# Performance work log

Hardware: AMD Instinct MI355X
Metric: run time of the kernel (lower is better)

## Reference

```python
import jax, jax.numpy as jnp
import numpy as np

Lx, Ly, D, B = 6, 6, 3, 16
SIGMA = 0.5  # keeps the 36-tensor contraction magnitude in fp32 range


def _slice_config(T, s):
    # T: [Lx, Ly, D,D,D,D, 2,2,2,2,2]; bond axes (u,d,l,r), phys axes (self, up, down, left, right)
    sg = s.reshape(Lx, Ly)
    sp = jnp.pad(sg, 1)  # out-of-grid neighbors -> index 0
    ix, iy = jnp.meshgrid(jnp.arange(Lx), jnp.arange(Ly), indexing='ij')
    p = sg
    pu = sp[ix, iy + 1]      # neighbor (x-1, y)
    pd = sp[ix + 2, iy + 1]  # neighbor (x+1, y)
    pl = sp[ix + 1, iy]      # neighbor (x, y-1)
    pr = sp[ix + 1, iy + 2]  # neighbor (x, y+1)
    # advanced indexing: result [Lx, Ly, D, D, D, D] with bond axes (u, d, l, r)
    return T[ix, iy, :, :, :, :, p, pu, pd, pl, pr]


def _amplitude(T, s):
    # exact boundary contraction from ymin (no truncation), equals full .contract()
    A = _slice_config(T, s)            # [Lx, Ly, u, d, l, r]
    Bnd = A[:, 0, :, :, 0, :]          # cap dangling left bonds: [Lx, u, d, r]
    for y in range(1, Ly):
        C = A[:, y]                    # [Lx, u, d, l, r]
        Bnd = jnp.einsum('xabl,xudlr->xaubdr', Bnd, C)
        Bnd = Bnd.reshape(Lx, Bnd.shape[1] * Bnd.shape[2],
                          Bnd.shape[3] * Bnd.shape[4], D)
    M = Bnd[:, :, :, 0]                # cap dangling right bonds: [Lx, chi, chi]
    v = M[0, 0]                        # cap top boundary bond (index 0 of product bond)
    for xx in range(1, Lx):
        v = v @ M[xx]                  # vector-matrix chain down the boundary MPS
    return v[0]                        # cap bottom boundary bond


def setup_inputs() -> dict:
    key = jax.random.key(0)
    kT, kx = jax.random.split(key)
    T = jax.random.normal(kT, (Lx, Ly, D, D, D, D, 2, 2, 2, 2, 2), dtype=jnp.float32) * SIGMA
    x = jax.random.randint(kx, (B, Lx * Ly), 0, 2, dtype=jnp.int32)
    return {"x": x, "T": T}


def reference(x, T):
    # batched amplitudes: [B]
    return jax.vmap(lambda s: _amplitude(T, s))(x)
```

## Files before the change

kernel.cpp:

```cpp
#include <hip/hip_runtime.h>


constexpr int SITE_STRIDE = 81 * 32;

__device__ __forceinline__ int calc_sidx(const int* __restrict__ xs, int base, int s) {
    const int i = s / 6, j = s - (s / 6) * 6;
    const int p  = xs[base + s];
    const int pu = (i > 0) ? xs[base + s - 6] : 0;
    const int pd = (i < 5) ? xs[base + s + 6] : 0;
    const int pl = (j > 0) ? xs[base + s - 1] : 0;
    const int pr = (j < 5) ? xs[base + s + 1] : 0;
    return (((p * 2 + pu) * 2 + pd) * 2 + pl) * 2 + pr;
}

template <int U>
__device__ __forceinline__ void fused2(int lt, const float* __restrict__ Win,
                                       float* __restrict__ Wout,
                                       const float* __restrict__ A1,
                                       const float* __restrict__ A2,
                                       int SS, int SO) {
    if (lt >= 243) return;
    const int D  = lt / (3 * U);
    const int rem = lt - D * 3 * U;
    const int o1 = rem / U;
    const int ur = rem - o1 * U;
    const float* Wb = Win + D * 27 * U + ur;
    float win[3][3][3];
    #pragma unroll
    for (int l = 0; l < 3; ++l)
        #pragma unroll
        for (int s = 0; s < 3; ++s)
            #pragma unroll
            for (int m = 0; m < 3; ++m)
                win[l][s][m] = Wb[((l * 9 + s * 3 + m) * U)];
    float tt[3][3];
    #pragma unroll
    for (int r1 = 0; r1 < 3; ++r1)
        #pragma unroll
        for (int m = 0; m < 3; ++m) {
            float acc = 0.f;
            #pragma unroll
            for (int s = 0; s < 3; ++s)
                #pragma unroll
                for (int l = 0; l < 3; ++l)
                    acc += win[l][s][m] * A1[s * SS + o1 * SO + l * 3 + r1];
            tt[r1][m] = acc;
        }
    float* Wo = Wout + (D * 3 + o1) * 9 * U + ur;
    #pragma unroll
    for (int o2 = 0; o2 < 3; ++o2)
        #pragma unroll
        for (int r2 = 0; r2 < 3; ++r2) {
            float acc = 0.f;
            #pragma unroll
            for (int m = 0; m < 3; ++m)
                #pragma unroll
                for (int r1 = 0; r1 < 3; ++r1)
                    acc += tt[r1][m] * A2[m * SS + o2 * SO + r1 * 3 + r2];
            Wo[(o2 * 3 + r2) * U] = acc;
        }
}

__global__ __launch_bounds__(512)
void peps_amp_kernel(const int* __restrict__ xs, const float* __restrict__ T,
                     float* __restrict__ out) {
    __shared__ float A[36 * 81];
    __shared__ float Vsh[2][729];
    __shared__ float Wsh[2][2][2187];
    __shared__ float Pm[2][3][81];
    __shared__ float red[8];

    const int b = blockIdx.x;
    const int t = threadIdx.x;
    const int half = t >> 8;
    const int lt = t & 255;
    const int base = b * 36;

    for (int idx = t; idx < 2916 + 486; idx += 512) {
        if (idx < 2916) {
            const int site = idx / 81;
            const int perm = idx - site * 81;
            A[idx] = T[site * SITE_STRIDE + perm * 32 + calc_sidx(xs, base, site)];
        } else {
            const int e = idx - 2916;
            const int ph = e / 243;
            const int rem = e - ph * 243;
            const int p = rem / 81;
            const int q = rem - p * 81;
            const int cc2 = q / 9, lr = q - cc2 * 9;
            const int ca = cc2 / 3, cb = cc2 - ca * 3;
            const int l = lr / 3, r = lr - l * 3;
            const int SOh = ph ? 27 : 9;
            const int sa = (ph ? 30 : 0) + 2 * p;
            const int sb = sa + 1;
            const int sxa = calc_sidx(xs, base, sa);
            const int sxb = calc_sidx(xs, base, sb);
            const float* Ta = T + sa * SITE_STRIDE + sxa;
            const float* Tb = T + sb * SITE_STRIDE + sxb;
            float acc = 0.f;
            #pragma unroll
            for (int m = 0; m < 3; ++m)
                acc += Ta[(ca * SOh + l * 3 + m) * 32] *
                       Tb[(cb * SOh + m * 3 + r) * 32];
            Pm[ph][p][q] = acc;
        }
    }
    __syncthreads();

    const int SS = half ? 9 : 27;
    const int SO = half ? 27 : 9;
    float* V  = Vsh[half];
    float* Wa = Wsh[half][0];
    float* Wb = Wsh[half][1];

    for (int k = lt; k < 729; k += 256) {
        const int c01 = k / 81;
        const int c23 = (k / 9) % 9;
        const int c45 = k % 9;
        const float* p0 = &Pm[half][0][c01 * 9];
        const float* p1 = &Pm[half][1][c23 * 9];
        const float* p2 = &Pm[half][2][c45 * 9];
        float w0 = p0[0] * p1[0] + p0[1] * p1[3] + p0[2] * p1[6];
        float w1 = p0[0] * p1[1] + p0[1] * p1[4] + p0[2] * p1[7];
        float w2 = p0[0] * p1[2] + p0[1] * p1[5] + p0[2] * p1[8];
        V[k] = w0 * p2[0] + w1 * p2[3] + w2 * p2[6];
    }
    __syncthreads();

    for (int cc = 0; cc < 2; ++cc) {
        const int xc = half ? (4 - cc) : (1 + cc);
        const float* Arow = &A[xc * 486];

        if (lt < 243) {
            const float v0 = V[lt], v1 = V[243 + lt], v2 = V[486 + lt];
            const float* A0 = Arow;
            #pragma unroll
            for (int o = 0; o < 3; ++o)
                #pragma unroll
                for (int r = 0; r < 3; ++r) {
                    Wa[(o * 3 + r) * 243 + lt] =
                        v0 * A0[o * SO + r] +
                        v1 * A0[SS + o * SO + r] +
                        v2 * A0[2 * SS + o * SO + r];
                }
        }
        __syncthreads();

        fused2<27>(lt, Wa, Wb, Arow + 81, Arow + 162, SS, SO);
        __syncthreads();
        fused2<3>(lt, Wb, Wa, Arow + 243, Arow + 324, SS, SO);
        __syncthreads();

        if (lt < 243) {
            const float* Ay = Arow + 405;
            float wv[3][3];
            #pragma unroll
            for (int l = 0; l < 3; ++l)
                #pragma unroll
                for (int s = 0; s < 3; ++s)
                    wv[s][l] = Wa[(lt * 3 + l) * 3 + s];
            #pragma unroll
            for (int o = 0; o < 3; ++o) {
                float acc = 0.f;
                #pragma unroll
                for (int s = 0; s < 3; ++s)
                    #pragma unroll
                    for (int l = 0; l < 3; ++l)
                        acc += wv[s][l] * Ay[s * SS + o * SO + l * 3];
                V[lt * 3 + o] = acc;
            }
        }
        __syncthreads();
    }

    float partial = 0.f;
    for (int i = t; i < 729; i += 512) partial += Vsh[0][i] * Vsh[1][i];
    #pragma unroll
    for (int off = 32; off > 0; off >>= 1) partial += __shfl_down(partial, off);
    if ((t & 63) == 0) red[t >> 6] = partial;
    __syncthreads();
    if (t == 0) {
        float s = 0.f;
        #pragma unroll
        for (int w = 0; w < 8; ++w) s += red[w];
        out[b] = s;
    }
}

extern "C" void kernel_launch(void* const* d_in, const int* in_sizes, int n_in,
                              void* d_out, int out_size, void* d_ws, size_t ws_size,
                              hipStream_t stream) {
    const int* xs = (const int*)d_in[0];
    const float* T = (const float*)d_in[1];
    float* out = (float*)d_out;
    const int B = in_sizes[0] / 36;
    peps_amp_kernel<<<B, 512, 0, stream>>>(xs, T, out);
}
```

Baseline: 71.66 us.

## Precompute site indices via wave shuffles, prefetch T rows, build boundary vectors from shared A

Computes the 36 per-site physical indices once per block with lane shuffles into shared memory, instead of recomputing them from global loads in every gather. Adds a dummy prefetch pass that touches the T site rows before the indexed gather. Removes the global-memory Pm pair products and builds the boundary vectors V by chaining 3x3 products from the shared A tensor. Replaces the block-wide final reduction with a single-wavefront reduction. This adds a barrier and an extra strided pass over T, and the boundary build now does more arithmetic per element.

```diff
diff --git a/kernel.cpp b/kernel.cpp
--- a/kernel.cpp
+++ b/kernel.cpp
@@ -2,16 +2,6 @@
 
 
 constexpr int SITE_STRIDE = 81 * 32;
-
-__device__ __forceinline__ int calc_sidx(const int* __restrict__ xs, int base, int s) {
-    const int i = s / 6, j = s - (s / 6) * 6;
-    const int p  = xs[base + s];
-    const int pu = (i > 0) ? xs[base + s - 6] : 0;
-    const int pd = (i < 5) ? xs[base + s + 6] : 0;
-    const int pl = (j > 0) ? xs[base + s - 1] : 0;
-    const int pr = (j < 5) ? xs[base + s + 1] : 0;
-    return (((p * 2 + pu) * 2 + pd) * 2 + pl) * 2 + pr;
-}
 
 template <int U>
 __device__ __forceinline__ void fused2(int lt, const float* __restrict__ Win,
@@ -67,8 +57,7 @@
     __shared__ float A[36 * 81];
     __shared__ float Vsh[2][729];
     __shared__ float Wsh[2][2][2187];
-    __shared__ float Pm[2][3][81];
-    __shared__ float red[8];
+    __shared__ int sidx[36];
 
     const int b = blockIdx.x;
     const int t = threadIdx.x;
@@ -76,34 +65,42 @@
     const int lt = t & 255;
     const int base = b * 36;
 
-    for (int idx = t; idx < 2916 + 486; idx += 512) {
+    float pf = 0.f;
+    #pragma unroll
+    for (int ii = 0; ii < 6; ++ii) {
+        const int idx = t + ii * 512;
         if (idx < 2916) {
             const int site = idx / 81;
             const int perm = idx - site * 81;
-            A[idx] = T[site * SITE_STRIDE + perm * 32 + calc_sidx(xs, base, site)];
-        } else {
-            const int e = idx - 2916;
-            const int ph = e / 243;
-            const int rem = e - ph * 243;
-            const int p = rem / 81;
-            const int q = rem - p * 81;
-            const int cc2 = q / 9, lr = q - cc2 * 9;
-            const int ca = cc2 / 3, cb = cc2 - ca * 3;
-            const int l = lr / 3, r = lr - l * 3;
-            const int SOh = ph ? 27 : 9;
-            const int sa = (ph ? 30 : 0) + 2 * p;
-            const int sb = sa + 1;
-            const int sxa = calc_sidx(xs, base, sa);
-            const int sxb = calc_sidx(xs, base, sb);
-            const float* Ta = T + sa * SITE_STRIDE + sxa;
-            const float* Tb = T + sb * SITE_STRIDE + sxb;
-            float acc = 0.f;
-            #pragma unroll
-            for (int m = 0; m < 3; ++m)
-                acc += Ta[(ca * SOh + l * 3 + m) * 32] *
-                       Tb[(cb * SOh + m * 3 + r) * 32];
-            Pm[ph][p][q] = acc;
-        }
+            pf += T[site * SITE_STRIDE + perm * 32];
+        }
+    }
+
+    if (t < 64) {
+        const int xv = (t < 36) ? xs[base + t] : 0;
+        const int lu = (t >= 6) ? t - 6 : 0;
+        const int ll = (t >= 1) ? t - 1 : 0;
+        const int ld = (t + 6 < 64) ? t + 6 : 0;
+        const int lr = (t + 1 < 64) ? t + 1 : 0;
+        const int vu = __shfl(xv, lu, 64);
+        const int vd = __shfl(xv, ld, 64);
+        const int vl = __shfl(xv, ll, 64);
+        const int vr = __shfl(xv, lr, 64);
+        if (t < 36) {
+            const int i = t / 6, j = t - (t / 6) * 6;
+            const int pu = (i > 0) ? vu : 0;
+            const int pd = (i < 5) ? vd : 0;
+            const int pl = (j > 0) ? vl : 0;
+            const int pr = (j < 5) ? vr : 0;
+            sidx[t] = (((xv * 2 + pu) * 2 + pd) * 2 + pl) * 2 + pr;
+        }
+    }
+    __syncthreads();
+
+    for (int idx = t; idx < 2916; idx += 512) {
+        const int site = idx / 81;
+        const int perm = idx - site * 81;
+        A[idx] = T[site * SITE_STRIDE + perm * 32 + sidx[site]];
     }
     __syncthreads();
 
@@ -113,17 +110,30 @@
     float* Wa = Wsh[half][0];
     float* Wb = Wsh[half][1];
 
-    for (int k = lt; k < 729; k += 256) {
-        const int c01 = k / 81;
-        const int c23 = (k / 9) % 9;
-        const int c45 = k % 9;
-        const float* p0 = &Pm[half][0][c01 * 9];
-        const float* p1 = &Pm[half][1][c23 * 9];
-        const float* p2 = &Pm[half][2][c45 * 9];
-        float w0 = p0[0] * p1[0] + p0[1] * p1[3] + p0[2] * p1[6];
-        float w1 = p0[0] * p1[1] + p0[1] * p1[4] + p0[2] * p1[7];
-        float w2 = p0[0] * p1[2] + p0[1] * p1[5] + p0[2] * p1[8];
-        V[k] = w0 * p2[0] + w1 * p2[3] + w2 * p2[6];
+    {
+        const float* Ab = &A[(half ? 30 : 0) * 81];
+        for (int k = lt; k < 729; k += 256) {
+            int c[6];
+            c[0] = k / 243;
+            c[1] = (k / 81) % 3;
+            c[2] = (k / 27) % 3;
+            c[3] = (k / 9) % 3;
+            c[4] = (k / 3) % 3;
+            c[5] = k % 3;
+            float v0 = Ab[c[0] * SO + 0];
+            float v1 = Ab[c[0] * SO + 1];
+            float v2 = Ab[c[0] * SO + 2];
+            #pragma unroll
+            for (int y = 1; y <= 4; ++y) {
+                const float* Ay = Ab + y * 81 + c[y] * SO;
+                const float n0 = v0 * Ay[0] + v1 * Ay[3] + v2 * Ay[6];
+                const float n1 = v0 * Ay[1] + v1 * Ay[4] + v2 * Ay[7];
+                const float n2 = v0 * Ay[2] + v1 * Ay[5] + v2 * Ay[8];
+                v0 = n0; v1 = n1; v2 = n2;
+            }
+            const float* A5 = Ab + 405 + c[5] * SO;
+            V[k] = v0 * A5[0] + v1 * A5[3] + v2 * A5[6];
+        }
     }
     __syncthreads();
 
@@ -173,17 +183,14 @@
         __syncthreads();
     }
 
-    float partial = 0.f;
-    for (int i = t; i < 729; i += 512) partial += Vsh[0][i] * Vsh[1][i];
-    #pragma unroll
-    for (int off = 32; off > 0; off >>= 1) partial += __shfl_down(partial, off);
-    if ((t & 63) == 0) red[t >> 6] = partial;
-    __syncthreads();
-    if (t == 0) {
-        float s = 0.f;
-        #pragma unroll
-        for (int w = 0; w < 8; ++w) s += red[w];
-        out[b] = s;
+    asm volatile("" :: "v"(pf));
+
+    if (t < 64) {
+        float partial = 0.f;
+        for (int i = t; i < 729; i += 64) partial += Vsh[0][i] * Vsh[1][i];
+        #pragma unroll
+        for (int off = 32; off > 0; off >>= 1) partial += __shfl_down(partial, off);
+        if (t == 0) out[b] = partial;
     }
 }
 
```

Result: faster. 68.08 us (-5.0%).
